# Kernel optimization log

Measured on AMD Instinct MI355X. Metric: run time of the kernel, lower is better.

## Reference

```python
import jax, jax.numpy as jnp
import numpy as np

EMBED_DIM = 1024
NUM_HEADS = 16
HEAD_DIM = 64
B, S = 4, 2048


def setup_inputs() -> dict:
    key = jax.random.key(0)
    ks = jax.random.split(key, 5)
    std = 0.02
    x = jax.random.normal(ks[0], (B, S, EMBED_DIM), dtype=jnp.float32)
    Wq = std * jax.random.normal(ks[1], (NUM_HEADS, EMBED_DIM, HEAD_DIM), dtype=jnp.float32)
    Wk = std * jax.random.normal(ks[2], (NUM_HEADS, EMBED_DIM, HEAD_DIM), dtype=jnp.float32)
    Wv = std * jax.random.normal(ks[3], (NUM_HEADS, EMBED_DIM, HEAD_DIM), dtype=jnp.float32)
    Wo = std * jax.random.normal(ks[4], (NUM_HEADS, HEAD_DIM, EMBED_DIM), dtype=jnp.float32)
    bq = jnp.zeros((NUM_HEADS, HEAD_DIM), dtype=jnp.float32)
    bk = jnp.zeros((NUM_HEADS, HEAD_DIM), dtype=jnp.float32)
    bv = jnp.zeros((NUM_HEADS, HEAD_DIM), dtype=jnp.float32)
    bo = jnp.zeros((EMBED_DIM,), dtype=jnp.float32)
    return {"x": x, "Wq": Wq, "bq": bq, "Wk": Wk, "bk": bk,
            "Wv": Wv, "bv": bv, "Wo": Wo, "bo": bo}


def reference(x, Wq, bq, Wk, bk, Wv, bv, Wo, bo):
    # q,k,v: [b, s, n, h]
    q = jnp.einsum('bsd,ndh->bsnh', x, Wq) + bq
    k = jnp.einsum('bsd,ndh->bsnh', x, Wk) + bk
    v = jnp.einsum('bsd,ndh->bsnh', x, Wv) + bv
    scale = 1.0 / (HEAD_DIM ** 0.5)
    # non-causal full attention matrix [b, n, s, t]
    attn = jnp.einsum('bsnh,btnh->bnst', q, k) * scale
    attn = jax.nn.softmax(attn, axis=-1)
    after = jnp.einsum('bnst,btnh->bsnh', attn, v)
    out = jnp.einsum('bsnh,nhd->bsd', after, Wo) + bo
    return out
```

## Files before the change

### kernel.cpp

```cpp
#include <hip/hip_runtime.h>

typedef __bf16 bf16;
typedef bf16 bf16x8 __attribute__((ext_vector_type(8)));
typedef bf16 bf16x4 __attribute__((ext_vector_type(4)));
typedef bf16 bf16x2 __attribute__((ext_vector_type(2)));
typedef float f32x4 __attribute__((ext_vector_type(4)));
typedef float f32x16 __attribute__((ext_vector_type(16)));
typedef unsigned int u32;
typedef u32 u32x4 __attribute__((ext_vector_type(4)));
typedef int i32x2 __attribute__((ext_vector_type(2)));

constexpr int Bb = 4, Ss = 2048, Dd = 1024, NH = 16, HD = 64;
constexpr int BS = Bb * Ss;
constexpr float CSC = 0.18033688011112042f;

__device__ __forceinline__ int sw(int row, int col) {
  return (row << 6) + (col ^ ((row & 7) << 3));
}
__device__ __forceinline__ int sw128(int row, int col) {
  return (row << 7) + (col ^ ((row & 7) << 3));
}

__device__ __forceinline__ void g2l16(const bf16* g, bf16* l) {
  __builtin_amdgcn_global_load_lds(
      (const __attribute__((address_space(1))) void*)g,
      (__attribute__((address_space(3))) void*)l, 16, 0, 0);
}

__device__ __forceinline__ u32 pkbf(float a, float b) {
  bf16x2 v = {(bf16)a, (bf16)b};
  return __builtin_bit_cast(u32, v);
}

__global__ void prep(const float* __restrict__ x, bf16* __restrict__ xb,
                     const float* __restrict__ Wq, const float* __restrict__ Wk,
                     const float* __restrict__ Wv, const float* __restrict__ Wo,
                     const float* __restrict__ bq, const float* __restrict__ bk,
                     const float* __restrict__ bv,
                     bf16* __restrict__ WT_all, bf16* __restrict__ WoT,
                     float* __restrict__ bias_all) {
  __shared__ bf16 Ts[64 * 72];
  const int t = threadIdx.x;
  if (blockIdx.y == 0) {
    int o = (blockIdx.x * 256 + t) * 4;
    f32x4 v = *(const f32x4*)&x[o];
    bf16x4 r = {(bf16)v[0], (bf16)v[1], (bf16)v[2], (bf16)v[3]};
    *(bf16x4*)&xb[o] = r;
    return;
  }
  if (blockIdx.x > 1024) return;
  if (blockIdx.x == 1024) {
    for (int j = t; j < 3072; j += 256) {
      int s2 = j >> 10;
      const float* bb = (s2 == 0) ? bq : (s2 == 1) ? bk : bv;
      bias_all[j] = bb[j & 1023] * (s2 == 0 ? CSC : 1.0f);
    }
    return;
  }
  const int sel = blockIdx.x >> 8, bx = blockIdx.x & 255;
  if (sel < 3) {
    const float* W = (sel == 0) ? Wq : (sel == 1) ? Wk : Wv;
    float scale = (sel == 0) ? CSC : 1.0f;
    int head = bx >> 4, dt = bx & 15;
    const float* src = W + head * 65536 + dt * 64 * 64;
#pragma unroll
    for (int i = 0; i < 4; ++i) {
      int idx = i * 256 + t;
      int dr = idx >> 4, hc = (idx & 15) * 4;
      f32x4 v = *(const f32x4*)&src[dr * 64 + hc];
#pragma unroll
      for (int k = 0; k < 4; ++k) Ts[(hc + k) * 72 + dr] = (bf16)(v[k] * scale);
    }
    __syncthreads();
    bf16* dst = WT_all + (size_t)sel * 1048576 + (size_t)(head * 64) * 1024 + dt * 64;
#pragma unroll
    for (int i = 0; i < 2; ++i) {
      int idx = i * 256 + t;
      int hr = idx >> 3, ch = (idx & 7) * 8;
      *(bf16x8*)&dst[(size_t)hr * 1024 + ch] = *(const bf16x8*)&Ts[hr * 72 + ch];
    }
  } else {
    int ct = bx >> 4, dt = bx & 15;
    const float* src = Wo + (size_t)(ct * 64) * 1024 + dt * 64;
#pragma unroll
    for (int i = 0; i < 4; ++i) {
      int idx = i * 256 + t;
      int cr = idx >> 4, dc = (idx & 15) * 4;
      f32x4 v = *(const f32x4*)&src[(size_t)cr * 1024 + dc];
#pragma unroll
      for (int k = 0; k < 4; ++k) Ts[(dc + k) * 72 + cr] = (bf16)v[k];
    }
    __syncthreads();
    bf16* dst = WoT + (size_t)(dt * 64) * 1024 + ct * 64;
#pragma unroll
    for (int i = 0; i < 2; ++i) {
      int idx = i * 256 + t;
      int dr = idx >> 3, ch = (idx & 7) * 8;
      *(bf16x8*)&dst[(size_t)dr * 1024 + ch] = *(const bf16x8*)&Ts[dr * 72 + ch];
    }
  }
}

__device__ __forceinline__ void gemm_core(const bf16* __restrict__ A,
                                          const bf16* __restrict__ BT,
                                          int m0, int n0, bf16* As, bf16* Bs,
                                          f32x4 (&acc)[4][4]) {
  const int t = threadIdx.x;
  const int l = t & 63, q = l >> 4, lm = l & 15;
  const int w = t >> 6, wm = w & 1, wn = w >> 1;
  int ro[4], co[4];
#pragma unroll
  for (int i = 0; i < 4; ++i) {
    int o = i * 256 + t;
    ro[i] = o >> 3;
    co[i] = ((o & 7) ^ ((o >> 3) & 7)) << 3;
  }
  const int lbase = (t & 192) * 8;
  for (int k0 = 0; k0 < 1024; k0 += 64) {
    __syncthreads();
#pragma unroll
    for (int i = 0; i < 4; ++i)
      g2l16(&A[(size_t)(m0 + ro[i]) * 1024 + k0 + co[i]], &As[i * 2048 + lbase]);
#pragma unroll
    for (int i = 0; i < 4; ++i)
      g2l16(&BT[(size_t)(n0 + ro[i]) * 1024 + k0 + co[i]], &Bs[i * 2048 + lbase]);
    __syncthreads();
#pragma unroll
    for (int kh = 0; kh < 2; ++kh) {
      bf16x8 a[4], b[4];
#pragma unroll
      for (int i = 0; i < 4; ++i)
        a[i] = *(const bf16x8*)&As[sw(wm * 64 + i * 16 + lm, kh * 32 + q * 8)];
#pragma unroll
      for (int i = 0; i < 4; ++i)
        b[i] = *(const bf16x8*)&Bs[sw(wn * 64 + i * 16 + lm, kh * 32 + q * 8)];
#pragma unroll
      for (int mt = 0; mt < 4; ++mt)
#pragma unroll
        for (int nt = 0; nt < 4; ++nt)
          acc[mt][nt] = __builtin_amdgcn_mfma_f32_16x16x32_bf16(a[mt], b[nt], acc[mt][nt], 0, 0, 0);
    }
  }
}

__global__ __launch_bounds__(256) void gemm_qkv(const bf16* __restrict__ xb,
                                                const bf16* __restrict__ WT,
                                                const float* __restrict__ bias_all,
                                                bf16* __restrict__ QKb,
                                                bf16* __restrict__ VTb) {
  __shared__ __align__(16) bf16 SMEM[2 * 128 * 64];
  bf16* As = SMEM;
  bf16* Bs = SMEM + 128 * 64;
  const int bid = blockIdx.x;
  const int t = threadIdx.x;
  const int l = t & 63, q = l >> 4, lm = l & 15;
  const int w = t >> 6, wm = w & 1, wn = w >> 1;
  const bool vmode = bid >= 1024;
  int m0, n0;
  const bf16 *A, *BT;
  if (!vmode) {
    int xcd = bid & 7, idx = bid >> 3;
    m0 = (idx >> 1) * 128;
    n0 = (xcd * 2 + (idx & 1)) * 128;
    A = xb; BT = WT;
  } else {
    int b2 = bid - 1024;
    int xcd = b2 & 7, idx = b2 >> 3;
    m0 = (idx >> 3) * 128;
    n0 = (xcd * 8 + (idx & 7)) * 128;
    A = WT + (size_t)2048 * 1024; BT = xb;
  }
  f32x4 acc[4][4] = {};
  gemm_core(A, BT, m0, n0, As, Bs, acc);
  if (vmode) {
    __syncthreads();
#pragma unroll
    for (int nt = 0; nt < 4; ++nt) {
      int sl = wn * 64 + nt * 16 + lm;
#pragma unroll
      for (int mt = 0; mt < 4; ++mt) {
        int ml = wm * 64 + mt * 16 + q * 4;
#pragma unroll
        for (int r = 0; r < 4; ++r)
          SMEM[sw128(ml + r, sl)] = (bf16)(acc[mt][nt][r] + bias_all[2048 + m0 + ml + r]);
      }
    }
    __syncthreads();
    int hh = t >> 1, half = (t & 1) * 64;
    int m = m0 + hh;
    size_t gb = (size_t)((n0 >> 11) * 16 + (m >> 6)) * 131072 +
                (size_t)(m & 63) * 2048 + (n0 & 2047) + half;
#pragma unroll
    for (int k = 0; k < 8; ++k)
      *(bf16x8*)&VTb[gb + k * 8] = *(const bf16x8*)&SMEM[sw128(hh, half + k * 8)];
  } else {
#pragma unroll
    for (int nt = 0; nt < 4; ++nt) {
      int col = n0 + wn * 64 + nt * 16 + lm;
      float bb = bias_all[col];
#pragma unroll
      for (int mt = 0; mt < 4; ++mt) {
        int row = m0 + wm * 64 + mt * 16 + q * 4;
#pragma unroll
        for (int r = 0; r < 4; ++r)
          QKb[(size_t)(row + r) * 2048 + col] = (bf16)(acc[mt][nt][r] + bb);
      }
    }
  }
}

__global__ __launch_bounds__(256) void gemm_out(const bf16* __restrict__ after,
                                                const bf16* __restrict__ WoT,
                                                const float* __restrict__ bo,
                                                float* __restrict__ out) {
  __shared__ __align__(16) bf16 SMEM[2 * 128 * 64];
  const int bid = blockIdx.x;
  const int t = threadIdx.x;
  const int l = t & 63, q = l >> 4, lm = l & 15;
  const int w = t >> 6, wm = w & 1, wn = w >> 1;
  const int xcd = bid & 7, idx = bid >> 3;
  const int n0 = xcd * 128, m0 = idx * 128;
  f32x4 acc[4][4] = {};
  gemm_core(after, WoT, m0, n0, SMEM, SMEM + 128 * 64, acc);
#pragma unroll
  for (int nt = 0; nt < 4; ++nt) {
    int col = n0 + wn * 64 + nt * 16 + lm;
    float bb = bo[col];
#pragma unroll
    for (int mt = 0; mt < 4; ++mt) {
      int row = m0 + wm * 64 + mt * 16 + q * 4;
#pragma unroll
      for (int r = 0; r < 4; ++r)
        out[(size_t)(row + r) * 1024 + col] = acc[mt][nt][r] + bb;
    }
  }
}

__global__ __launch_bounds__(256, 4) void attn(const bf16* __restrict__ QK,
                                               const bf16* __restrict__ VT,
                                               bf16* __restrict__ after) {
  __shared__ __align__(16) bf16 Ks[2][64 * 64];
  __shared__ __align__(16) bf16 Vs[2][64 * 64];
  const int t = threadIdx.x;
  const int l = t & 63, w = t >> 6;
  const int lh = l & 31, H = l >> 5;
  const int f = blockIdx.x;
  const int bn = (f & 7) | ((f >> 7) << 3);
  const int s0 = ((f >> 3) & 15) * 128;
  const int b = bn >> 4, n = bn & 15;
  const bf16* Qb = QK + (size_t)(b * 2048) * 2048 + n * 64;
  const bf16* Kb = Qb + 1024;
  const bf16* Vtb = VT + (size_t)bn * 131072;
  int ro[4], co[4];
#pragma unroll
  for (int i = 0; i < 4; ++i) {
    int o = i * 256 + t;
    ro[i] = o >> 3;
    co[i] = ((o & 7) ^ ((o >> 3) & 7)) << 3;
  }
  const int lbase = (t & 192) * 8;
  bf16* Kflat = &Ks[0][0];
#pragma unroll
  for (int i = 0; i < 4; ++i)
    g2l16(&Qb[(size_t)(s0 + ro[i]) * 2048 + co[i]], Kflat + i * 2048 + lbase);
  __syncthreads();
  bf16x8 qb[4];
#pragma unroll
  for (int ks = 0; ks < 4; ++ks)
    qb[ks] = *(const bf16x8*)&Kflat[sw(w * 32 + lh, ks * 16 + H * 8)];
  __syncthreads();
#pragma unroll
  for (int i = 0; i < 2; ++i) {
    g2l16(&Kb[(size_t)ro[i] * 2048 + co[i]], &Ks[0][i * 2048 + lbase]);
    g2l16(&Vtb[(size_t)ro[i] * 2048 + co[i]], &Vs[0][i * 2048 + lbase]);
  }
  f32x16 o_acc[2] = {};
  float rs = 0.f;
  for (int rd = 0; rd < 32; ++rd) {
    const int cur = rd & 1;
    __syncthreads();
    if (rd < 31) {
      int t0n = (rd + 1) * 64, nb = cur ^ 1;
#pragma unroll
      for (int i = 0; i < 2; ++i) {
        g2l16(&Kb[(size_t)(t0n + ro[i]) * 2048 + co[i]], &Ks[nb][i * 2048 + lbase]);
        g2l16(&Vtb[(size_t)ro[i] * 2048 + t0n + co[i]], &Vs[nb][i * 2048 + lbase]);
      }
    }
#pragma unroll
    for (int tt = 0; tt < 2; ++tt) {
      f32x16 sc = {};
#pragma unroll
      for (int ks = 0; ks < 4; ++ks) {
        bf16x8 kb = *(const bf16x8*)&Ks[cur][sw(tt * 32 + lh, ks * 16 + H * 8)];
        sc = __builtin_amdgcn_mfma_f32_32x32x16_bf16(kb, qb[ks], sc, 0, 0, 0);
      }
      u32 pk[8];
#pragma unroll
      for (int i = 0; i < 8; ++i) {
        float p0 = __builtin_amdgcn_exp2f(sc[2 * i]);
        float p1 = __builtin_amdgcn_exp2f(sc[2 * i + 1]);
        rs += p0 + p1;
        pk[i] = pkbf(p0, p1);
      }
#pragma unroll
      for (int ks2 = 0; ks2 < 2; ++ks2) {
        u32x4 av;
#if __has_builtin(__builtin_amdgcn_permlane32_swap)
        i32x2 sA = __builtin_amdgcn_permlane32_swap((int)pk[ks2 * 4 + 0], (int)pk[ks2 * 4 + 2],
                                                    false, false);
        i32x2 sB = __builtin_amdgcn_permlane32_swap((int)pk[ks2 * 4 + 1], (int)pk[ks2 * 4 + 3],
                                                    false, false);
        av[0] = (u32)sA[0]; av[1] = (u32)sB[0]; av[2] = (u32)sA[1]; av[3] = (u32)sB[1];
#else
        u32 xx[4];
        xx[0] = __shfl_xor((int)pk[ks2 * 4 + 0], 32);
        xx[1] = __shfl_xor((int)pk[ks2 * 4 + 1], 32);
        xx[2] = __shfl_xor((int)pk[ks2 * 4 + 2], 32);
        xx[3] = __shfl_xor((int)pk[ks2 * 4 + 3], 32);
        av[0] = H ? xx[2] : pk[ks2 * 4 + 0];
        av[1] = H ? xx[3] : pk[ks2 * 4 + 1];
        av[2] = H ? pk[ks2 * 4 + 2] : xx[0];
        av[3] = H ? pk[ks2 * 4 + 3] : xx[1];
#endif
        bf16x8 pa = __builtin_bit_cast(bf16x8, av);
#pragma unroll
        for (int ht = 0; ht < 2; ++ht) {
          bf16x8 vb = *(const bf16x8*)&Vs[cur][sw(ht * 32 + lh, tt * 32 + ks2 * 16 + H * 8)];
          o_acc[ht] = __builtin_amdgcn_mfma_f32_32x32x16_bf16(pa, vb, o_acc[ht], 0, 0, 0);
        }
      }
    }
  }
  rs += __shfl_xor(rs, 32);
  float inv = 1.f / rs;
#pragma unroll
  for (int r = 0; r < 16; ++r) {
    int sl = (r & 3) + 8 * (r >> 2) + 4 * H;
    float invr = __shfl(inv, sl);
    size_t base = (size_t)(b * 2048 + s0 + w * 32 + sl) * 1024 + n * 64;
#pragma unroll
    for (int ht = 0; ht < 2; ++ht)
      after[base + ht * 32 + lh] = (bf16)(o_acc[ht][r] * invr);
  }
}

extern "C" void kernel_launch(void* const* d_in, const int* in_sizes, int n_in,
                              void* d_out, int out_size, void* d_ws, size_t ws_size,
                              hipStream_t stream) {
  const float* x  = (const float*)d_in[0];
  const float* Wq = (const float*)d_in[1];
  const float* bq = (const float*)d_in[2];
  const float* Wk = (const float*)d_in[3];
  const float* bk = (const float*)d_in[4];
  const float* Wv = (const float*)d_in[5];
  const float* bv = (const float*)d_in[6];
  const float* Wo = (const float*)d_in[7];
  const float* bo = (const float*)d_in[8];
  float* out = (float*)d_out;

  bf16* WT_all    = (bf16*)d_ws;
  bf16* WoT       = WT_all + (size_t)3072 * 1024;
  float* bias_all = (float*)(WoT + (size_t)1024 * 1024);
  bf16* xb        = (bf16*)(bias_all + 4096);
  bf16* QKb       = xb + (size_t)BS * Dd;
  bf16* VTb       = QKb + (size_t)BS * 2048;
  bf16* after     = VTb + (size_t)Bb * NH * HD * Ss;

  prep<<<dim3(8192, 2), dim3(256), 0, stream>>>(x, xb, Wq, Wk, Wv, Wo, bq, bk, bv,
                                                WT_all, WoT, bias_all);
  gemm_qkv<<<dim3(1536), dim3(256), 0, stream>>>(xb, WT_all, bias_all, QKb, VTb);
  attn<<<dim3(1024), dim3(256), 0, stream>>>(QKb, VTb, after);
  gemm_out<<<dim3(512), dim3(256), 0, stream>>>(after, WoT, bo, out);
}
```

Baseline: 283.3 us.

## Process two query tiles per wave in attention to reuse K/V fragments

```diff
diff --git a/kernel.cpp b/kernel.cpp
--- a/kernel.cpp
+++ b/kernel.cpp
@@ -236,112 +236,132 @@
   }
 }
 
-__global__ __launch_bounds__(256, 4) void attn(const bf16* __restrict__ QK,
+__global__ __launch_bounds__(256, 2) void attn(const bf16* __restrict__ QK,
                                                const bf16* __restrict__ VT,
                                                bf16* __restrict__ after) {
-  __shared__ __align__(16) bf16 Ks[2][64 * 64];
-  __shared__ __align__(16) bf16 Vs[2][64 * 64];
+  __shared__ __align__(16) bf16 SMEM[16384];
   const int t = threadIdx.x;
   const int l = t & 63, w = t >> 6;
   const int lh = l & 31, H = l >> 5;
   const int f = blockIdx.x;
-  const int bn = (f & 7) | ((f >> 7) << 3);
-  const int s0 = ((f >> 3) & 15) * 128;
+  const int bn = (f & 7) | ((f >> 6) << 3);
+  const int s0 = ((f >> 3) & 7) * 256;
   const int b = bn >> 4, n = bn & 15;
   const bf16* Qb = QK + (size_t)(b * 2048) * 2048 + n * 64;
   const bf16* Kb = Qb + 1024;
   const bf16* Vtb = VT + (size_t)bn * 131072;
-  int ro[4], co[4];
-#pragma unroll
-  for (int i = 0; i < 4; ++i) {
-    int o = i * 256 + t;
-    ro[i] = o >> 3;
-    co[i] = ((o & 7) ^ ((o >> 3) & 7)) << 3;
-  }
+  const int rr = t >> 3;
+  const int co0 = ((t & 7) ^ (rr & 7)) << 3;
   const int lbase = (t & 192) * 8;
-  bf16* Kflat = &Ks[0][0];
-#pragma unroll
-  for (int i = 0; i < 4; ++i)
-    g2l16(&Qb[(size_t)(s0 + ro[i]) * 2048 + co[i]], Kflat + i * 2048 + lbase);
+#pragma unroll
+  for (int i = 0; i < 8; ++i)
+    g2l16(&Qb[(size_t)(s0 + i * 32 + rr) * 2048 + co0], &SMEM[i * 2048 + lbase]);
   __syncthreads();
-  bf16x8 qb[4];
-#pragma unroll
-  for (int ks = 0; ks < 4; ++ks)
-    qb[ks] = *(const bf16x8*)&Kflat[sw(w * 32 + lh, ks * 16 + H * 8)];
+  bf16x8 qb[2][4];
+#pragma unroll
+  for (int qt = 0; qt < 2; ++qt)
+#pragma unroll
+    for (int ks = 0; ks < 4; ++ks)
+      qb[qt][ks] = *(const bf16x8*)&SMEM[sw(w * 64 + qt * 32 + lh, ks * 16 + H * 8)];
   __syncthreads();
 #pragma unroll
   for (int i = 0; i < 2; ++i) {
-    g2l16(&Kb[(size_t)ro[i] * 2048 + co[i]], &Ks[0][i * 2048 + lbase]);
-    g2l16(&Vtb[(size_t)ro[i] * 2048 + co[i]], &Vs[0][i * 2048 + lbase]);
-  }
-  f32x16 o_acc[2] = {};
-  float rs = 0.f;
+    g2l16(&Kb[(size_t)(i * 32 + rr) * 2048 + co0], &SMEM[i * 2048 + lbase]);
+    g2l16(&Vtb[(size_t)(i * 32 + rr) * 2048 + co0], &SMEM[8192 + i * 2048 + lbase]);
+  }
+  f32x16 o_acc[2][2] = {};
+  float rsA[2] = {0.f, 0.f}, rsB[2] = {0.f, 0.f};
   for (int rd = 0; rd < 32; ++rd) {
     const int cur = rd & 1;
+    bf16* Ks = &SMEM[cur * 4096];
+    bf16* Vs = &SMEM[8192 + cur * 4096];
     __syncthreads();
     if (rd < 31) {
       int t0n = (rd + 1) * 64, nb = cur ^ 1;
 #pragma unroll
       for (int i = 0; i < 2; ++i) {
-        g2l16(&Kb[(size_t)(t0n + ro[i]) * 2048 + co[i]], &Ks[nb][i * 2048 + lbase]);
-        g2l16(&Vtb[(size_t)ro[i] * 2048 + t0n + co[i]], &Vs[nb][i * 2048 + lbase]);
+        g2l16(&Kb[(size_t)(t0n + i * 32 + rr) * 2048 + co0],
+              &SMEM[nb * 4096 + i * 2048 + lbase]);
+        g2l16(&Vtb[(size_t)(i * 32 + rr) * 2048 + t0n + co0],
+              &SMEM[8192 + nb * 4096 + i * 2048 + lbase]);
       }
     }
 #pragma unroll
     for (int tt = 0; tt < 2; ++tt) {
-      f32x16 sc = {};
-#pragma unroll
-      for (int ks = 0; ks < 4; ++ks) {
-        bf16x8 kb = *(const bf16x8*)&Ks[cur][sw(tt * 32 + lh, ks * 16 + H * 8)];
-        sc = __builtin_amdgcn_mfma_f32_32x32x16_bf16(kb, qb[ks], sc, 0, 0, 0);
+      bf16x8 kb[4];
+#pragma unroll
+      for (int ks = 0; ks < 4; ++ks)
+        kb[ks] = *(const bf16x8*)&Ks[sw(tt * 32 + lh, ks * 16 + H * 8)];
+      f32x16 sc[2] = {};
+      __builtin_amdgcn_s_setprio(1);
+#pragma unroll
+      for (int ks = 0; ks < 4; ++ks)
+#pragma unroll
+        for (int qt = 0; qt < 2; ++qt)
+          sc[qt] = __builtin_amdgcn_mfma_f32_32x32x16_bf16(kb[ks], qb[qt][ks], sc[qt], 0, 0, 0);
+      __builtin_amdgcn_s_setprio(0);
+      u32 pk[2][8];
+#pragma unroll
+      for (int qt = 0; qt < 2; ++qt)
+#pragma unroll
+        for (int i = 0; i < 8; ++i) {
+          float p0 = __builtin_amdgcn_exp2f(sc[qt][2 * i]);
+          float p1 = __builtin_amdgcn_exp2f(sc[qt][2 * i + 1]);
+          rsA[qt] += p0;
+          rsB[qt] += p1;
+          pk[qt][i] = pkbf(p0, p1);
+        }
+#pragma unroll
+      for (int ks2 = 0; ks2 < 2; ++ks2) {
+        bf16x8 pa[2];
+#pragma unroll
+        for (int qt = 0; qt < 2; ++qt) {
+          u32x4 av;
+#if __has_builtin(__builtin_amdgcn_permlane32_swap)
+          i32x2 sA = __builtin_amdgcn_permlane32_swap(
+              (int)pk[qt][ks2 * 4 + 0], (int)pk[qt][ks2 * 4 + 2], false, false);
+          i32x2 sB = __builtin_amdgcn_permlane32_swap(
+              (int)pk[qt][ks2 * 4 + 1], (int)pk[qt][ks2 * 4 + 3], false, false);
+          av[0] = (u32)sA[0]; av[1] = (u32)sB[0]; av[2] = (u32)sA[1]; av[3] = (u32)sB[1];
+#else
+          u32 xx[4];
+          xx[0] = __shfl_xor((int)pk[qt][ks2 * 4 + 0], 32);
+          xx[1] = __shfl_xor((int)pk[qt][ks2 * 4 + 1], 32);
+          xx[2] = __shfl_xor((int)pk[qt][ks2 * 4 + 2], 32);
+          xx[3] = __shfl_xor((int)pk[qt][ks2 * 4 + 3], 32);
+          av[0] = H ? xx[2] : pk[qt][ks2 * 4 + 0];
+          av[1] = H ? xx[3] : pk[qt][ks2 * 4 + 1];
+          av[2] = H ? pk[qt][ks2 * 4 + 2] : xx[0];
+          av[3] = H ? pk[qt][ks2 * 4 + 3] : xx[1];
+#endif
+          pa[qt] = __builtin_bit_cast(bf16x8, av);
+        }
+        __builtin_amdgcn_s_setprio(1);
+#pragma unroll
+        for (int ht = 0; ht < 2; ++ht) {
+          bf16x8 vb = *(const bf16x8*)&Vs[sw(ht * 32 + lh, tt * 32 + ks2 * 16 + H * 8)];
+#pragma unroll
+          for (int qt = 0; qt < 2; ++qt)
+            o_acc[qt][ht] = __builtin_amdgcn_mfma_f32_32x32x16_bf16(pa[qt], vb, o_acc[qt][ht], 0, 0, 0);
+        }
+        __builtin_amdgcn_s_setprio(0);
       }
-      u32 pk[8];
-#pragma unroll
-      for (int i = 0; i < 8; ++i) {
-        float p0 = __builtin_amdgcn_exp2f(sc[2 * i]);
-        float p1 = __builtin_amdgcn_exp2f(sc[2 * i + 1]);
-        rs += p0 + p1;
-        pk[i] = pkbf(p0, p1);
-      }
-#pragma unroll
-      for (int ks2 = 0; ks2 < 2; ++ks2) {
-        u32x4 av;
-#if __has_builtin(__builtin_amdgcn_permlane32_swap)
-        i32x2 sA = __builtin_amdgcn_permlane32_swap((int)pk[ks2 * 4 + 0], (int)pk[ks2 * 4 + 2],
-                                                    false, false);
-        i32x2 sB = __builtin_amdgcn_permlane32_swap((int)pk[ks2 * 4 + 1], (int)pk[ks2 * 4 + 3],
-                                                    false, false);
-        av[0] = (u32)sA[0]; av[1] = (u32)sB[0]; av[2] = (u32)sA[1]; av[3] = (u32)sB[1];
-#else
-        u32 xx[4];
-        xx[0] = __shfl_xor((int)pk[ks2 * 4 + 0], 32);
-        xx[1] = __shfl_xor((int)pk[ks2 * 4 + 1], 32);
-        xx[2] = __shfl_xor((int)pk[ks2 * 4 + 2], 32);
-        xx[3] = __shfl_xor((int)pk[ks2 * 4 + 3], 32);
-        av[0] = H ? xx[2] : pk[ks2 * 4 + 0];
-        av[1] = H ? xx[3] : pk[ks2 * 4 + 1];
-        av[2] = H ? pk[ks2 * 4 + 2] : xx[0];
-        av[3] = H ? pk[ks2 * 4 + 3] : xx[1];
-#endif
-        bf16x8 pa = __builtin_bit_cast(bf16x8, av);
-#pragma unroll
-        for (int ht = 0; ht < 2; ++ht) {
-          bf16x8 vb = *(const bf16x8*)&Vs[cur][sw(ht * 32 + lh, tt * 32 + ks2 * 16 + H * 8)];
-          o_acc[ht] = __builtin_amdgcn_mfma_f32_32x32x16_bf16(pa, vb, o_acc[ht], 0, 0, 0);
-        }
-      }
-    }
-  }
-  rs += __shfl_xor(rs, 32);
-  float inv = 1.f / rs;
-#pragma unroll
-  for (int r = 0; r < 16; ++r) {
-    int sl = (r & 3) + 8 * (r >> 2) + 4 * H;
-    float invr = __shfl(inv, sl);
-    size_t base = (size_t)(b * 2048 + s0 + w * 32 + sl) * 1024 + n * 64;
-#pragma unroll
-    for (int ht = 0; ht < 2; ++ht)
-      after[base + ht * 32 + lh] = (bf16)(o_acc[ht][r] * invr);
+    }
+  }
+#pragma unroll
+  for (int qt = 0; qt < 2; ++qt) {
+    float rs = rsA[qt] + rsB[qt];
+    rs += __shfl_xor(rs, 32);
+    float inv = 1.f / rs;
+#pragma unroll
+    for (int r = 0; r < 16; ++r) {
+      int sl = (r & 3) + 8 * (r >> 2) + 4 * H;
+      float invr = __shfl(inv, sl);
+      size_t base = (size_t)(b * 2048 + s0 + w * 64 + qt * 32 + sl) * 1024 + n * 64;
+#pragma unroll
+      for (int ht = 0; ht < 2; ++ht)
+        after[base + ht * 32 + lh] = (bf16)(o_acc[qt][ht][r] * invr);
+    }
   }
 }
 
@@ -370,6 +390,6 @@
   prep<<<dim3(8192, 2), dim3(256), 0, stream>>>(x, xb, Wq, Wk, Wv, Wo, bq, bk, bv,
                                                 WT_all, WoT, bias_all);
   gemm_qkv<<<dim3(1536), dim3(256), 0, stream>>>(xb, WT_all, bias_all, QKb, VTb);
-  attn<<<dim3(1024), dim3(256), 0, stream>>>(QKb, VTb, after);
+  attn<<<dim3(512), dim3(256), 0, stream>>>(QKb, VTb, after);
   gemm_out<<<dim3(512), dim3(256), 0, stream>>>(after, WoT, bo, out);
 }
```

Result: faster. 276.5 us (-2.4%).
